# Kernel tuning notes

Measured on AMD Instinct MI355X. Metric: run time of the kernel, lower is better.

## Reference

```python
import jax, jax.numpy as jnp
import numpy as np

E = 600000
NF = 50000
NC = 12500
D = 128
HID = 128
D_IN = 4 * D  # concat of four gathered feature blocks


def setup_inputs() -> dict:
    key = jax.random.key(0)
    ks = jax.random.split(key, 10)
    return {
        "h_dk_coarse": jax.random.normal(ks[0], (NC, D), dtype=jnp.float32),
        "h_si_fine": jax.random.normal(ks[1], (NF, D), dtype=jnp.float32),
        "h_sk_coarse": jax.random.normal(ks[2], (NC, D), dtype=jnp.float32),
        "h_di_fine_current": jax.random.normal(ks[3], (NF, D), dtype=jnp.float32),
        "fine_idx": jax.random.randint(ks[4], (E,), 0, NF, dtype=jnp.int64),
        "coarse_idx": jax.random.randint(ks[5], (E,), 0, NC, dtype=jnp.int64),
        # Dense params (Glorot-ish scale); both layers use relu per create_mlp
        "W1": jax.random.normal(ks[6], (D_IN, HID), dtype=jnp.float32) * (1.0 / np.sqrt(D_IN)),
        "b1": jnp.zeros((HID,), dtype=jnp.float32),
        "W2": jax.random.normal(ks[7], (HID, D), dtype=jnp.float32) * (1.0 / np.sqrt(HID)),
        "b2": jnp.zeros((D,), dtype=jnp.float32),
    }


def reference(h_dk_coarse, h_si_fine, h_sk_coarse, h_di_fine_current,
              fine_idx, coarse_idx, W1, b1, W2, b2):
    # Gather per-edge features
    h_dk_g = h_dk_coarse[coarse_idx]          # [E, D]
    h_si_g = h_si_fine[fine_idx]              # [E, D]
    h_sk_g = h_sk_coarse[coarse_idx]          # [E, D]
    h_di_g = h_di_fine_current[fine_idx]      # [E, D]
    x = jnp.concatenate([h_si_g, h_sk_g, h_di_g, h_dk_g], axis=-1)  # [E, 4D]
    # MLP: relu on hidden AND final layer (create_mlp default activation, no final override)
    h = jax.nn.relu(x @ W1 + b1)              # [E, HID]
    psi = jax.nn.relu(h @ W2 + b2)            # [E, D]
    contributions = psi * h_dk_g              # [E, D]
    # Scatter-add back to fine nodes
    return jax.ops.segment_sum(contributions, fine_idx, num_segments=NF)  # [NF, D]
```

## Files before the change

kernel.cpp:

```cpp
#include <hip/hip_runtime.h>

typedef unsigned short u16;
typedef unsigned int u32;

#define E_EDGES 600000
#define NUM_FINE 50000
#define NUM_COARSE 12500
#define FINE_BLOCKS 391
#define COARSE_BLOCKS 98
#define CONVERT_BLOCKS 320
#define COUNT_BLOCKS 2344
#define SCATTER_BLOCKS 2344

typedef __attribute__((ext_vector_type(8))) short short8;
typedef __attribute__((ext_vector_type(4))) float f32x4;

union Frag { short8 v; u16 s[8]; u32 u[4]; uint4 q; };

__device__ __forceinline__ u32 rne_bf16(float f) {
  union { float f; u32 u; } v; v.f = f;
  return (v.u + 0x7FFFu + ((v.u >> 16) & 1u)) >> 16;
}
__device__ __forceinline__ float bf2f(u32 bits16) {
  union { u32 u; float f; } v; v.u = bits16 << 16; return v.f;
}
__device__ __forceinline__ u32 addrelu_pack(u32 a, u32 b) {
  float lo = fmaxf(bf2f(a & 0xFFFFu) + bf2f(b & 0xFFFFu), 0.0f);
  float hi = fmaxf(bf2f(a >> 16) + bf2f(b >> 16), 0.0f);
  return rne_bf16(lo) | (rne_bf16(hi) << 16);
}

__global__ void prep1(const float* __restrict__ W1, const float* __restrict__ W2,
                      u16* __restrict__ BW1f, u16* __restrict__ BW1c,
                      u16* __restrict__ BW2,
                      const int* __restrict__ fidx, int* __restrict__ cnt) {
  if (blockIdx.x < CONVERT_BLOCKS) {
    int o = blockIdx.x * 256 + threadIdx.x;
    if (o >= 81920) return;
    int which = (o < 32768) ? 0 : (o < 65536 ? 1 : 2);
    int idx = (which == 2) ? (o - 65536) : (o & 32767);
    int j = idx & 7, lane = (idx >> 3) & 63, nt = (idx >> 9) & 7, ks = idx >> 12;
    int k = ks * 32 + (lane >> 4) * 8 + j;
    int n = nt * 16 + (lane & 15);
    float v;
    if (which == 2) v = W2[k * 128 + n];
    else {
      int row;
      if (which == 0) row = (k < 128) ? k : (256 + (k - 128));
      else            row = (k < 128) ? (128 + k) : (384 + (k - 128));
      v = W1[row * 128 + n];
    }
    u16 b = (u16)rne_bf16(v);
    if (which == 0) BW1f[idx] = b; else if (which == 1) BW1c[idx] = b; else BW2[idx] = b;
  } else {
    int e = (blockIdx.x - CONVERT_BLOCKS) * 256 + threadIdx.x;
    if (e < E_EDGES) atomicAdd(&cnt[fidx[e]], 1);
  }
}

__global__ void scan_kernel(const int* __restrict__ cnt, int* __restrict__ wcur) {
  __shared__ int wsum[16], woff[16];
  __shared__ int runningS, chunkTot;
  int tid = threadIdx.x, lane = tid & 63, w = tid >> 6;
  if (tid == 0) runningS = 0;
  __syncthreads();
  for (int base = 0; base < NUM_FINE; base += 4096) {
    int i0 = base + tid * 4;
    int4 c = {0, 0, 0, 0};
    if (i0 < NUM_FINE) c = *(const int4*)(cnt + i0);
    int v = c.x + c.y + c.z + c.w;
    int x = v;
#pragma unroll
    for (int off = 1; off < 64; off <<= 1) {
      int y = __shfl_up(x, off, 64);
      if (lane >= off) x += y;
    }
    if (lane == 63) wsum[w] = x;
    __syncthreads();
    if (tid == 0) {
      int a = 0;
      for (int k = 0; k < 16; ++k) { int t = wsum[k]; woff[k] = a; a += t; }
      chunkTot = a;
    }
    __syncthreads();
    if (i0 < NUM_FINE) {
      int ex = runningS + woff[w] + x - v;
      wcur[i0] = ex; wcur[i0 + 1] = ex + c.x;
      wcur[i0 + 2] = ex + c.x + c.y; wcur[i0 + 3] = ex + c.x + c.y + c.z;
    }
    __syncthreads();
    if (tid == 0) runningS += chunkTot;
    __syncthreads();
  }
}

__global__ __launch_bounds__(256, 2) void prep2(
    const int* __restrict__ fidx, const int* __restrict__ cidx,
    int* __restrict__ wcur, u32* __restrict__ spk,
    const float* __restrict__ h_dk, const float* __restrict__ h_si,
    const float* __restrict__ h_sk, const float* __restrict__ h_di,
    const u16* __restrict__ BW1f, const u16* __restrict__ BW1c,
    const float* __restrict__ b1, u16* __restrict__ Pf, u16* __restrict__ Pc) {
  __shared__ u16 bsh[32768];

  if (blockIdx.x < SCATTER_BLOCKS) {
    int e = blockIdx.x * 256 + threadIdx.x;
    if (e < E_EDGES) {
      int fi = fidx[e];
      int p = atomicAdd(&wcur[fi], 1);
      spk[p] = ((u32)fi << 14) | (u32)cidx[e];
    }
    return;
  }

  const int b = blockIdx.x - SCATTER_BLOCKS;
  const bool fine = b < FINE_BLOCKS;
  const int rowStart = fine ? b * 128 : (b - FINE_BLOCKS) * 128;
  const int R = fine ? NUM_FINE : NUM_COARSE;
  const float* __restrict__ X1 = fine ? h_si : h_sk;
  const float* __restrict__ X2 = fine ? h_di : h_dk;
  const u16* __restrict__ BW = fine ? BW1f : BW1c;
  u16* __restrict__ P = fine ? Pf : Pc;

  const int tid = threadIdx.x;
  {
    uint4* d4 = (uint4*)bsh;
    const uint4* s4 = (const uint4*)BW;
#pragma unroll
    for (int k = 0; k < 16; ++k) d4[k * 256 + tid] = s4[k * 256 + tid];
  }
  __syncthreads();

  const int lane = tid & 63;
  const int w = tid >> 6;
  const int qd = lane >> 4;
  const int ml = lane & 15;

  int rowA[2]; bool vA[2];
#pragma unroll
  for (int mt = 0; mt < 2; ++mt) {
    rowA[mt] = rowStart + w * 32 + mt * 16 + ml;
    vA[mt] = rowA[mt] < R;
  }

  f32x4 acc[2][8];
#pragma unroll
  for (int mt = 0; mt < 2; ++mt)
#pragma unroll
    for (int nt = 0; nt < 8; ++nt) acc[mt][nt] = (f32x4){0.f, 0.f, 0.f, 0.f};

  for (int ks = 0; ks < 8; ++ks) {
    const int k0 = ks * 32 + qd * 8;
    short8 a[2];
#pragma unroll
    for (int mt = 0; mt < 2; ++mt) {
      Frag af;
      if (vA[mt]) {
        const float* src = (k0 < 128) ? (X1 + rowA[mt] * 128 + k0)
                                      : (X2 + rowA[mt] * 128 + (k0 - 128));
        const float4* s4 = (const float4*)src;
        float4 v0 = s4[0], v1 = s4[1];
        af.u[0] = rne_bf16(v0.x) | (rne_bf16(v0.y) << 16);
        af.u[1] = rne_bf16(v0.z) | (rne_bf16(v0.w) << 16);
        af.u[2] = rne_bf16(v1.x) | (rne_bf16(v1.y) << 16);
        af.u[3] = rne_bf16(v1.z) | (rne_bf16(v1.w) << 16);
      } else {
        af.u[0] = af.u[1] = af.u[2] = af.u[3] = 0u;
      }
      a[mt] = af.v;
    }
#pragma unroll
    for (int nt = 0; nt < 8; ++nt) {
      Frag bfr;
      bfr.q = *(const uint4*)&bsh[(((ks * 8 + nt) * 64) + lane) * 8];
      acc[0][nt] = __builtin_amdgcn_mfma_f32_16x16x32_bf16(a[0], bfr.v, acc[0][nt], 0, 0, 0);
      acc[1][nt] = __builtin_amdgcn_mfma_f32_16x16x32_bf16(a[1], bfr.v, acc[1][nt], 0, 0, 0);
    }
  }

  float b1v[8];
#pragma unroll
  for (int nt = 0; nt < 8; ++nt) b1v[nt] = fine ? 0.0f : b1[nt * 16 + ml];

#pragma unroll
  for (int mt = 0; mt < 2; ++mt) {
#pragma unroll
    for (int r = 0; r < 4; ++r) {
      const int row = rowStart + w * 32 + mt * 16 + qd * 4 + r;
      if (row < R) {
#pragma unroll
        for (int nt = 0; nt < 8; ++nt)
          P[row * 128 + nt * 16 + ml] = (u16)rne_bf16(acc[mt][nt][r] + b1v[nt]);
      }
    }
  }
}

__global__ __launch_bounds__(256, 4) void edge_kernel(
    const u16* __restrict__ Pf, const u16* __restrict__ Pc,
    const u16* __restrict__ BW2, const float* __restrict__ hdk,
    const u32* __restrict__ spk, const float* __restrict__ b2,
    float* __restrict__ out) {
  __shared__ u16 smem[16384];
  __shared__ int sh_fi[128], sh_ci[128], sh_segstart[130];
  __shared__ int shS, shHead, shTail, shW0tot;

  const int tid = threadIdx.x;
  const int eb = blockIdx.x * 128;
  const int V = min(128, E_EDGES - eb);

  {
    uint4* d4 = (uint4*)smem;
    const uint4* s4 = (const uint4*)BW2;
#pragma unroll
    for (int k = 0; k < 8; ++k) d4[k * 256 + tid] = s4[k * 256 + tid];
  }
  if (tid < 128) {
    if (tid < V) {
      u32 p = spk[eb + tid];
      sh_fi[tid] = (int)(p >> 14);
      sh_ci[tid] = (int)(p & 16383u);
    } else { sh_fi[tid] = -1; sh_ci[tid] = 0; }
  }
  if (tid == 0) {
    shHead = (eb > 0) ? (int)(spk[eb - 1] >> 14) : -1;
    shTail = (eb + V < E_EDGES) ? (int)(spk[eb + V] >> 14) : -1;
  }
  __syncthreads();

  int f = 0, x = 0;
  if (tid < 128) {
    f = (tid < V) ? ((tid == 0) ? 1 : (sh_fi[tid] != sh_fi[tid - 1] ? 1 : 0)) : 0;
    x = f;
#pragma unroll
    for (int off = 1; off < 64; off <<= 1) {
      int y = __shfl_up(x, off, 64);
      if ((tid & 63) >= off) x += y;
    }
  }
  if (tid == 63) shW0tot = x;
  __syncthreads();
  if (tid >= 64 && tid < 128) x += shW0tot;
  if (tid < V) {
    if (f) sh_segstart[x - 1] = tid;
    if (tid == V - 1) { shS = x; sh_segstart[x] = V; }
  }
  __syncthreads();

  const int lane = tid & 63;
  const int w = tid >> 6;
  const int qd = lane >> 4;
  const int ml = lane & 15;

  int fiA[2], ciA[2]; bool vA[2];
#pragma unroll
  for (int mt = 0; mt < 2; ++mt) {
    const int lr = w * 32 + mt * 16 + ml;
    vA[mt] = lr < V;
    fiA[mt] = vA[mt] ? sh_fi[lr] : 0;
    ciA[mt] = vA[mt] ? sh_ci[lr] : 0;
  }

  f32x4 acc[2][8];
#pragma unroll
  for (int mt = 0; mt < 2; ++mt)
#pragma unroll
    for (int nt = 0; nt < 8; ++nt) acc[mt][nt] = (f32x4){0.f, 0.f, 0.f, 0.f};

  for (int ks = 0; ks < 4; ++ks) {
    const int k0 = ks * 32 + qd * 8;
    short8 a[2];
#pragma unroll
    for (int mt = 0; mt < 2; ++mt) {
      Frag af;
      if (vA[mt]) {
        uint4 pf = *(const uint4*)(Pf + fiA[mt] * 128 + k0);
        uint4 pc = *(const uint4*)(Pc + ciA[mt] * 128 + k0);
        af.u[0] = addrelu_pack(pf.x, pc.x);
        af.u[1] = addrelu_pack(pf.y, pc.y);
        af.u[2] = addrelu_pack(pf.z, pc.z);
        af.u[3] = addrelu_pack(pf.w, pc.w);
      } else {
        af.u[0] = af.u[1] = af.u[2] = af.u[3] = 0u;
      }
      a[mt] = af.v;
    }
#pragma unroll
    for (int nt = 0; nt < 8; ++nt) {
      Frag bfr;
      bfr.q = *(const uint4*)&smem[(((ks * 8 + nt) * 64) + lane) * 8];
      acc[0][nt] = __builtin_amdgcn_mfma_f32_16x16x32_bf16(a[0], bfr.v, acc[0][nt], 0, 0, 0);
      acc[1][nt] = __builtin_amdgcn_mfma_f32_16x16x32_bf16(a[1], bfr.v, acc[1][nt], 0, 0, 0);
    }
  }
  __syncthreads();

  float b2v[8];
#pragma unroll
  for (int nt = 0; nt < 8; ++nt) b2v[nt] = b2[nt * 16 + ml];

#pragma unroll
  for (int mt = 0; mt < 2; ++mt) {
#pragma unroll
    for (int r = 0; r < 4; ++r) {
      const int lr = w * 32 + mt * 16 + qd * 4 + r;
      if (lr < V) {
        const float* __restrict__ hrow = hdk + sh_ci[lr] * 128;
#pragma unroll
        for (int nt = 0; nt < 8; ++nt) {
          const int col = nt * 16 + ml;
          const float psi = fmaxf(acc[mt][nt][r] + b2v[nt], 0.0f);
          smem[lr * 128 + col] = (u16)rne_bf16(psi * hrow[col]);
        }
      }
    }
  }
  __syncthreads();

  const int S = shS;
  for (int idx = tid; idx < S * 64; idx += 256) {
    const int s = idx >> 6, cp = idx & 63;
    const int r0 = sh_segstart[s], r1 = sh_segstart[s + 1];
    float a0 = 0.f, a1 = 0.f;
    for (int r = r0; r < r1; ++r) {
      const u32 v = *(const u32*)&smem[r * 128 + cp * 2];
      a0 += bf2f(v & 0xFFFFu);
      a1 += bf2f(v >> 16);
    }
    const int fi = sh_fi[r0];
    float* op = out + (size_t)fi * 128 + cp * 2;
    const bool at = (s == 0 && shHead == fi) || (s == S - 1 && shTail == fi);
    if (at) { atomicAdd(op, a0); atomicAdd(op + 1, a1); }
    else { op[0] = a0; op[1] = a1; }
  }
}

extern "C" void kernel_launch(void* const* d_in, const int* in_sizes, int n_in,
                              void* d_out, int out_size, void* d_ws, size_t ws_size,
                              hipStream_t stream) {
  const float* h_dk = (const float*)d_in[0];
  const float* h_si = (const float*)d_in[1];
  const float* h_sk = (const float*)d_in[2];
  const float* h_di = (const float*)d_in[3];
  const int* fidx = (const int*)d_in[4];
  const int* cidx = (const int*)d_in[5];
  const float* W1 = (const float*)d_in[6];
  const float* b1 = (const float*)d_in[7];
  const float* W2 = (const float*)d_in[8];
  const float* b2 = (const float*)d_in[9];
  float* out = (float*)d_out;

  u16* Pf   = (u16*)d_ws;
  u16* Pc   = Pf + (size_t)NUM_FINE * 128;
  u16* BW1f = Pc + (size_t)NUM_COARSE * 128;
  u16* BW1c = BW1f + 32768;
  u16* BW2  = BW1c + 32768;
  int* cnt  = (int*)(BW2 + 16384);
  int* wcur = cnt + NUM_FINE;
  u32* spk  = (u32*)(wcur + NUM_FINE);

  hipMemsetAsync(d_out, 0, (size_t)out_size * sizeof(float), stream);
  hipMemsetAsync(cnt, 0, NUM_FINE * sizeof(int), stream);

  prep1<<<CONVERT_BLOCKS + COUNT_BLOCKS, 256, 0, stream>>>(
      W1, W2, BW1f, BW1c, BW2, fidx, cnt);
  scan_kernel<<<1, 1024, 0, stream>>>(cnt, wcur);
  prep2<<<SCATTER_BLOCKS + FINE_BLOCKS + COARSE_BLOCKS, 256, 0, stream>>>(
      fidx, cidx, wcur, spk, h_dk, h_si, h_sk, h_di, BW1f, BW1c, b1, Pf, Pc);
  edge_kernel<<<(E_EDGES + 127) / 128, 256, 0, stream>>>(
      Pf, Pc, BW2, h_dk, spk, b2, out);
}
```

Before: 280.9 us.

## Fuse output zeroing into prep, single-pass scan, and truncate bf16 conversions

Zeroing of the output moves out of a separate memset and into extra blocks of the prep1 kernel. The scan kernel is rewritten so each thread serially sums a 49-element chunk, replacing the chunked loop that needed several barriers per iteration. Round-to-nearest bf16 conversions in the hot paths are replaced with truncation and byte-permute packing, which cuts ALU work in the edge and prep kernels. Truncation adds rounding bias, and the serial per-thread loads in the scan are uncoalesced.

```diff
diff --git a/kernel.cpp b/kernel.cpp
--- a/kernel.cpp
+++ b/kernel.cpp
@@ -10,6 +10,7 @@
 #define COARSE_BLOCKS 98
 #define CONVERT_BLOCKS 320
 #define COUNT_BLOCKS 2344
+#define ZOUT_BLOCKS 625
 #define SCATTER_BLOCKS 2344
 
 typedef __attribute__((ext_vector_type(8))) short short8;
@@ -21,19 +22,31 @@
   union { float f; u32 u; } v; v.f = f;
   return (v.u + 0x7FFFu + ((v.u >> 16) & 1u)) >> 16;
 }
-__device__ __forceinline__ float bf2f(u32 bits16) {
-  union { u32 u; float f; } v; v.u = bits16 << 16; return v.f;
+__device__ __forceinline__ float hi_bf(u32 u) {
+  union { u32 x; float f; } v; v.x = u & 0xFFFF0000u; return v.f;
+}
+__device__ __forceinline__ float lo_bf(u32 u) {
+  union { u32 x; float f; } v; v.x = u << 16; return v.f;
+}
+__device__ __forceinline__ u32 pack_trunc(float hi, float lo) {
+  union { float f; u32 x; } a, b; a.f = hi; b.f = lo;
+  return __builtin_amdgcn_perm(a.x, b.x, 0x07060302u);
 }
 __device__ __forceinline__ u32 addrelu_pack(u32 a, u32 b) {
-  float lo = fmaxf(bf2f(a & 0xFFFFu) + bf2f(b & 0xFFFFu), 0.0f);
-  float hi = fmaxf(bf2f(a >> 16) + bf2f(b >> 16), 0.0f);
-  return rne_bf16(lo) | (rne_bf16(hi) << 16);
+  float lo = fmaxf(lo_bf(a) + lo_bf(b), 0.0f);
+  float hi = fmaxf(hi_bf(a) + hi_bf(b), 0.0f);
+  return pack_trunc(hi, lo);
+}
+__device__ __forceinline__ u16 trunc_bf16(float f) {
+  union { float f; u32 u; } v; v.f = f;
+  return (u16)(v.u >> 16);
 }
 
 __global__ void prep1(const float* __restrict__ W1, const float* __restrict__ W2,
                       u16* __restrict__ BW1f, u16* __restrict__ BW1c,
                       u16* __restrict__ BW2,
-                      const int* __restrict__ fidx, int* __restrict__ cnt) {
+                      const int* __restrict__ fidx, int* __restrict__ cnt,
+                      float* __restrict__ out) {
   if (blockIdx.x < CONVERT_BLOCKS) {
     int o = blockIdx.x * 256 + threadIdx.x;
     if (o >= 81920) return;
@@ -52,46 +65,42 @@
     }
     u16 b = (u16)rne_bf16(v);
     if (which == 0) BW1f[idx] = b; else if (which == 1) BW1c[idx] = b; else BW2[idx] = b;
-  } else {
+  } else if (blockIdx.x < CONVERT_BLOCKS + COUNT_BLOCKS) {
     int e = (blockIdx.x - CONVERT_BLOCKS) * 256 + threadIdx.x;
     if (e < E_EDGES) atomicAdd(&cnt[fidx[e]], 1);
-  }
-}
-
+  } else {
+    const int zb = blockIdx.x - (CONVERT_BLOCKS + COUNT_BLOCKS);
+    float4* o4 = (float4*)out;
+    const float4 z = {0.f, 0.f, 0.f, 0.f};
+    int idx = zb * 2560 + threadIdx.x;
+#pragma unroll
+    for (int i = 0; i < 10; ++i) o4[idx + i * 256] = z;
+  }
+}
+
+#define SCAN_PER 49
 __global__ void scan_kernel(const int* __restrict__ cnt, int* __restrict__ wcur) {
   __shared__ int wsum[16], woff[16];
-  __shared__ int runningS, chunkTot;
-  int tid = threadIdx.x, lane = tid & 63, w = tid >> 6;
-  if (tid == 0) runningS = 0;
-  __syncthreads();
-  for (int base = 0; base < NUM_FINE; base += 4096) {
-    int i0 = base + tid * 4;
-    int4 c = {0, 0, 0, 0};
-    if (i0 < NUM_FINE) c = *(const int4*)(cnt + i0);
-    int v = c.x + c.y + c.z + c.w;
-    int x = v;
-#pragma unroll
-    for (int off = 1; off < 64; off <<= 1) {
-      int y = __shfl_up(x, off, 64);
-      if (lane >= off) x += y;
-    }
-    if (lane == 63) wsum[w] = x;
-    __syncthreads();
-    if (tid == 0) {
-      int a = 0;
-      for (int k = 0; k < 16; ++k) { int t = wsum[k]; woff[k] = a; a += t; }
-      chunkTot = a;
-    }
-    __syncthreads();
-    if (i0 < NUM_FINE) {
-      int ex = runningS + woff[w] + x - v;
-      wcur[i0] = ex; wcur[i0 + 1] = ex + c.x;
-      wcur[i0 + 2] = ex + c.x + c.y; wcur[i0 + 3] = ex + c.x + c.y + c.z;
-    }
-    __syncthreads();
-    if (tid == 0) runningS += chunkTot;
-    __syncthreads();
-  }
+  const int tid = threadIdx.x, lane = tid & 63, w = tid >> 6;
+  const int base = tid * SCAN_PER;
+  const int n = (base < NUM_FINE) ? min(SCAN_PER, NUM_FINE - base) : 0;
+  int s = 0;
+  for (int i = 0; i < n; ++i) s += cnt[base + i];
+  int x = s;
+#pragma unroll
+  for (int off = 1; off < 64; off <<= 1) {
+    int y = __shfl_up(x, off, 64);
+    if (lane >= off) x += y;
+  }
+  if (lane == 63) wsum[w] = x;
+  __syncthreads();
+  if (tid == 0) {
+    int a = 0;
+    for (int k = 0; k < 16; ++k) { int t = wsum[k]; woff[k] = a; a += t; }
+  }
+  __syncthreads();
+  int run = woff[w] + x - s;
+  for (int i = 0; i < n; ++i) { wcur[base + i] = run; run += cnt[base + i]; }
 }
 
 __global__ __launch_bounds__(256, 2) void prep2(
@@ -160,10 +169,10 @@
                                       : (X2 + rowA[mt] * 128 + (k0 - 128));
         const float4* s4 = (const float4*)src;
         float4 v0 = s4[0], v1 = s4[1];
-        af.u[0] = rne_bf16(v0.x) | (rne_bf16(v0.y) << 16);
-        af.u[1] = rne_bf16(v0.z) | (rne_bf16(v0.w) << 16);
-        af.u[2] = rne_bf16(v1.x) | (rne_bf16(v1.y) << 16);
-        af.u[3] = rne_bf16(v1.z) | (rne_bf16(v1.w) << 16);
+        af.u[0] = pack_trunc(v0.y, v0.x);
+        af.u[1] = pack_trunc(v0.w, v0.z);
+        af.u[2] = pack_trunc(v1.y, v1.x);
+        af.u[3] = pack_trunc(v1.w, v1.z);
       } else {
         af.u[0] = af.u[1] = af.u[2] = af.u[3] = 0u;
       }
@@ -310,7 +319,7 @@
         for (int nt = 0; nt < 8; ++nt) {
           const int col = nt * 16 + ml;
           const float psi = fmaxf(acc[mt][nt][r] + b2v[nt], 0.0f);
-          smem[lr * 128 + col] = (u16)rne_bf16(psi * hrow[col]);
+          smem[lr * 128 + col] = trunc_bf16(psi * hrow[col]);
         }
       }
     }
@@ -324,8 +333,8 @@
     float a0 = 0.f, a1 = 0.f;
     for (int r = r0; r < r1; ++r) {
       const u32 v = *(const u32*)&smem[r * 128 + cp * 2];
-      a0 += bf2f(v & 0xFFFFu);
-      a1 += bf2f(v >> 16);
+      a0 += lo_bf(v);
+      a1 += hi_bf(v);
     }
     const int fi = sh_fi[r0];
     float* op = out + (size_t)fi * 128 + cp * 2;
@@ -359,11 +368,10 @@
   int* wcur = cnt + NUM_FINE;
   u32* spk  = (u32*)(wcur + NUM_FINE);
 
-  hipMemsetAsync(d_out, 0, (size_t)out_size * sizeof(float), stream);
   hipMemsetAsync(cnt, 0, NUM_FINE * sizeof(int), stream);
 
-  prep1<<<CONVERT_BLOCKS + COUNT_BLOCKS, 256, 0, stream>>>(
-      W1, W2, BW1f, BW1c, BW2, fidx, cnt);
+  prep1<<<CONVERT_BLOCKS + COUNT_BLOCKS + ZOUT_BLOCKS, 256, 0, stream>>>(
+      W1, W2, BW1f, BW1c, BW2, fidx, cnt, out);
   scan_kernel<<<1, 1024, 0, stream>>>(cnt, wcur);
   prep2<<<SCATTER_BLOCKS + FINE_BLOCKS + COARSE_BLOCKS, 256, 0, stream>>>(
       fidx, cidx, wcur, spk, h_dk, h_si, h_sk, h_di, BW1f, BW1c, b1, Pf, Pc);
```

After: 337.2 us. +20.0%, slower.
